# Optimization experiments

Measured on AMD Instinct MI355X. Metric: run time of the kernel, lower is better.

Reference implementation:

```python
import jax, jax.numpy as jnp
import numpy as np

KS = 3      # kernel_size
PAD = 1     # zero padding applied to x before sampling
STRIDE = 1  # stride of p_conv and final conv (as written in the repo)


def conv2d(x, w, b=None, stride=1, padding=0):
    out = jax.lax.conv_general_dilated(
        x, w, (stride, stride), [(padding, padding), (padding, padding)],
        dimension_numbers=("NCHW", "OIHW", "NCHW"))
    if b is not None:
        out = out + b[None, :, None, None]
    return out


def setup_inputs() -> dict:
    key = jax.random.key(0)
    k1, k2, k3, k4 = jax.random.split(key, 4)
    bsz, inc, outc, H, W = 4, 64, 128, 128, 128
    N = KS * KS
    x = jax.random.normal(k1, (bsz, inc, H, W), dtype=jnp.float32)
    # p_conv: Conv2d(inc, 2*ks*ks, 3, padding=1) with bias (small weights -> modest offsets)
    w_p = jax.random.normal(k2, (2 * N, inc, 3, 3), dtype=jnp.float32) * 0.02
    b_p = jax.random.normal(k3, (2 * N,), dtype=jnp.float32) * 0.1
    # final conv: Conv2d(inc, outc, ks, stride=stride, bias=None)
    w_conv = jax.random.normal(k4, (outc, inc, KS, KS), dtype=jnp.float32) * 0.05
    return {"x": x, "w_p": w_p, "b_p": b_p, "w_conv": w_conv}


def deform_conv_forward(x, w_p, b_p, w_conv):
    ks, pad, stride = KS, PAD, STRIDE
    offset = conv2d(x, w_p, b_p, stride=stride, padding=1)  # (b, 2N, oh, ow)
    N = offset.shape[1] // 2
    bsz, c, _, _ = x.shape
    oh, ow = offset.shape[2], offset.shape[3]
    xp = jnp.pad(x, ((0, 0), (0, 0), (pad, pad), (pad, pad)))
    Hp, Wp = xp.shape[2], xp.shape[3]

    # p_n: kernel-grid offsets, order matches torch.meshgrid 'ij' then flatten
    r = jnp.arange(-(ks - 1) // 2, (ks - 1) // 2 + 1, dtype=x.dtype)
    pnx, pny = jnp.meshgrid(r, r, indexing="ij")
    p_n = jnp.concatenate([pnx.ravel(), pny.ravel()])[None, :, None, None]  # (1,2N,1,1)

    # p_0: base sampling coordinates (1-indexed into padded image)
    i0 = jnp.arange(1, oh * stride + 1, stride, dtype=x.dtype)
    j0 = jnp.arange(1, ow * stride + 1, stride, dtype=x.dtype)
    p0x = jnp.broadcast_to(i0[:, None], (oh, ow))[None, None]
    p0y = jnp.broadcast_to(j0[None, :], (oh, ow))[None, None]
    p_0 = jnp.concatenate([jnp.tile(p0x, (1, N, 1, 1)), jnp.tile(p0y, (1, N, 1, 1))], axis=1)

    p = (p_0 + p_n + offset).transpose(0, 2, 3, 1)  # (b, oh, ow, 2N)

    q_lt_f = jnp.floor(p)
    q_rb_f = q_lt_f + 1.0

    def clamp_q(q):
        return jnp.concatenate(
            [jnp.clip(q[..., :N], 0, Hp - 1), jnp.clip(q[..., N:], 0, Wp - 1)],
            axis=-1).astype(jnp.int32)

    q_lt = clamp_q(q_lt_f)
    q_rb = clamp_q(q_rb_f)
    q_lb = jnp.concatenate([q_lt[..., :N], q_rb[..., N:]], axis=-1)
    q_rt = jnp.concatenate([q_rb[..., :N], q_lt[..., N:]], axis=-1)

    # clamp p itself (indices are detached in torch; gradients flow only through p here)
    p = jnp.concatenate(
        [jnp.clip(p[..., :N], 0, Hp - 1), jnp.clip(p[..., N:], 0, Wp - 1)], axis=-1)
    px, py = p[..., :N], p[..., N:]

    qf = lambda q: q.astype(x.dtype)
    g_lt = (1 + (qf(q_lt[..., :N]) - px)) * (1 + (qf(q_lt[..., N:]) - py))
    g_rb = (1 - (qf(q_rb[..., :N]) - px)) * (1 - (qf(q_rb[..., N:]) - py))
    g_lb = (1 + (qf(q_lb[..., :N]) - px)) * (1 - (qf(q_lb[..., N:]) - py))
    g_rt = (1 - (qf(q_rt[..., :N]) - px)) * (1 + (qf(q_rt[..., N:]) - py))

    x_flat = xp.reshape(bsz, c, Hp * Wp)

    def get_x_q(q):
        idx = q[..., :N] * Wp + q[..., N:]                     # (b, oh, ow, N)
        idxf = jnp.broadcast_to(idx.reshape(bsz, 1, -1), (bsz, c, oh * ow * N))
        return jnp.take_along_axis(x_flat, idxf, axis=2).reshape(bsz, c, oh, ow, N)

    x_off = (g_lt[:, None] * get_x_q(q_lt) + g_rb[:, None] * get_x_q(q_rb)
             + g_lb[:, None] * get_x_q(q_lb) + g_rt[:, None] * get_x_q(q_rt))

    # _reshape_x_offset: (b,c,oh,ow,ks*ks) -> (b,c,oh*ks,ow*ks)
    x_off = x_off.reshape(bsz, c, oh, ow, ks, ks).transpose(0, 1, 2, 4, 3, 5)
    x_off = x_off.reshape(bsz, c, oh * ks, ow * ks)

    return conv2d(x_off, w_conv, None, stride=stride, padding=0)


def reference(x, w_p, b_p, w_conv):
    return deform_conv_forward(x, w_p, b_p, w_conv)
```

## Files before the change

kernel.cpp:

```cpp
#include <hip/hip_runtime.h>
#include <hip/hip_bf16.h>

#define B_   4
#define IC   64
#define OC   128
#define HH   128
#define WW   128
#define HP   130
#define XOF  384
#define XPAD 388
#define OH2  382

typedef __attribute__((ext_vector_type(4))) float f32x4;
typedef __attribute__((ext_vector_type(8))) __bf16 bf16x8;
typedef __attribute__((ext_vector_type(8))) unsigned short us8;
typedef __attribute__((ext_vector_type(4), aligned(4))) float f32x4u;

__device__ __forceinline__ void gload16(const void* gsrc, void* ldst) {
    __builtin_amdgcn_global_load_lds(
        (const __attribute__((address_space(1))) void*)gsrc,
        (__attribute__((address_space(3))) void*)ldst, 16, 0, 0);
}

#define WAITV(N) asm volatile("s_waitcnt vmcnt(" #N ")" ::: "memory")

__device__ __forceinline__ float bf2f(unsigned short u) {
    union { unsigned int i; float f; } v; v.i = ((unsigned int)u) << 16; return v.f;
}
__device__ __forceinline__ unsigned short f2bf(float f) {
    __hip_bfloat16 h = __float2bfloat16(f);
    return reinterpret_cast<unsigned short&>(h);
}

__global__ __launch_bounds__(256) void prologue(const float* __restrict__ x,
                                                const float* __restrict__ w_p,
                                                const float* __restrict__ b_p,
                                                const float* __restrict__ wc,
                                                float* __restrict__ off,
                                                unsigned short* __restrict__ xt,
                                                unsigned short* __restrict__ Bt) {
    __shared__ __align__(16) char smem[18432];
    int bid = blockIdx.x;
    int tid = threadIdx.x;

    if (bid < 2048) {
        unsigned short (*tile)[34] = (unsigned short(*)[34])smem;
        int xt4 = bid & 3;
        int y   = (bid >> 2) & 127;
        int b   = bid >> 9;
        int x0  = xt4 * 32;

        int xl = tid & 31;
        int c8 = tid >> 5;
#pragma unroll
        for (int it = 0; it < 8; ++it) {
            int c = it * 8 + c8;
            tile[c][xl] = f2bf(x[(((size_t)b * IC + c) * HH + y) * WW + x0 + xl]);
        }
        __syncthreads();
        int c2 = (tid & 31) * 2;
#pragma unroll
        for (int it = 0; it < 4; ++it) {
            int xx = (tid >> 5) + it * 8;
            ushort2 v = { tile[c2][xx], tile[c2 + 1][xx] };
            *(ushort2*)(xt + (((size_t)b * HH + y) * WW + x0 + xx) * IC + c2) = v;
        }
    } else if (bid < 3072) {
        float (*part)[64][18] = (float(*)[64][18])smem;
        int obid = bid - 2048;
        int pxl = tid & 63;
        int icq = tid >> 6;
        int seg = obid & 1;
        int row = obid >> 1;
        int py  = row & 127;
        int b   = row >> 7;
        int px  = seg * 64 + pxl;
        int ic0 = __builtin_amdgcn_readfirstlane(icq << 4);

        float acc[18];
#pragma unroll
        for (int co = 0; co < 18; ++co) acc[co] = 0.f;

        const float* xb = x + ((size_t)b * IC + ic0) * HH * WW;

        for (int ci = 0; ci < 16; ++ci) {
            const float* xc = xb + (size_t)ci * HH * WW;
            float xv[9];
#pragma unroll
            for (int ky = 0; ky < 3; ++ky) {
                int yy = py + ky - 1;
                bool yok = (yy >= 0) && (yy < HH);
#pragma unroll
                for (int kx = 0; kx < 3; ++kx) {
                    int xx = px + kx - 1;
                    bool ok = yok && (xx >= 0) && (xx < WW);
                    xv[ky * 3 + kx] = ok ? xc[yy * WW + xx] : 0.f;
                }
            }
#pragma unroll
            for (int co = 0; co < 18; ++co) {
                const float* wrow = w_p + ((size_t)co * IC + ic0 + ci) * 9;
                f32x4u w0 = *(const f32x4u*)wrow;
                f32x4u w1 = *(const f32x4u*)(wrow + 4);
                float  w8 = wrow[8];
                acc[co] = fmaf(w0.x, xv[0], acc[co]);
                acc[co] = fmaf(w0.y, xv[1], acc[co]);
                acc[co] = fmaf(w0.z, xv[2], acc[co]);
                acc[co] = fmaf(w0.w, xv[3], acc[co]);
                acc[co] = fmaf(w1.x, xv[4], acc[co]);
                acc[co] = fmaf(w1.y, xv[5], acc[co]);
                acc[co] = fmaf(w1.z, xv[6], acc[co]);
                acc[co] = fmaf(w1.w, xv[7], acc[co]);
                acc[co] = fmaf(w8,   xv[8], acc[co]);
            }
        }

#pragma unroll
        for (int co = 0; co < 18; ++co) part[icq][pxl][co] = acc[co];
        __syncthreads();

        for (int co = icq; co < 18; co += 4) {
            float s = b_p[co] + part[0][pxl][co] + part[1][pxl][co]
                              + part[2][pxl][co] + part[3][pxl][co];
            off[((size_t)b * 18 + co) * HH * WW + (size_t)py * WW + px] = s;
        }
    } else {
        int t = (bid - 3072) * 256 + tid;
        if (t < 18 * 4 * 128 * 8) {
            int e  = t & 7;
            int oc = (t >> 3) & 127;
            int kg = (t >> 10) & 3;
            int s  = t >> 12;
            int ic = ((s & 1) << 5) + (kg << 3) + e;
            int kpos = s >> 1;
            int ky = kpos / 3, kx = kpos % 3;
            Bt[t] = f2bf(wc[(((size_t)oc * IC + ic) * 3 + ky) * 3 + kx]);
        }
    }
}

__global__ __launch_bounds__(256) void sample_nhwc(const unsigned short* __restrict__ xt,
                                                   const float* __restrict__ off,
                                                   unsigned short* __restrict__ xoff,
                                                   int b0, int nwg) {
    int orig = blockIdx.x;
    int chunk = nwg >> 3;
    int wg = (orig & 7) * chunk + (orig >> 3);

    int xtile = wg % 12;
    int tmp = wg / 12;
    int yy  = tmp % XOF;
    int bl  = tmp / XOF;
    int b   = b0 + bl;
    int xx0 = xtile * 32;

    int t  = threadIdx.x;
    int xl = t & 31;
    int cg = t >> 5;
    int xx = xx0 + xl;

    int j = xx / 3, kw = xx % 3;
    int i = yy / 3, kh = yy % 3;
    int n = kh * 3 + kw;

    const float* offb = off + (size_t)b * 18 * HH * WW + (size_t)i * WW + j;
    float offr = offb[(size_t)n * HH * WW];
    float offc = offb[(size_t)(n + 9) * HH * WW];

    float pr = (float)(i + kh) + offr;
    float pc = (float)(j + kw) + offc;

    float r0f = floorf(pr), c0f = floorf(pc);
    int r0 = min(max((int)r0f, 0), HP - 1);
    int c0 = min(max((int)c0f, 0), HP - 1);
    int r1 = min(max((int)(r0f + 1.f), 0), HP - 1);
    int c1 = min(max((int)(c0f + 1.f), 0), HP - 1);

    float prc = fminf(fmaxf(pr, 0.f), (float)(HP - 1));
    float pcc = fminf(fmaxf(pc, 0.f), (float)(HP - 1));

    float R0 = 1.f + ((float)r0 - prc);
    float R1 = 1.f - ((float)r1 - prc);
    float C0 = 1.f + ((float)c0 - pcc);
    float C1 = 1.f - ((float)c1 - pcc);

    int rr0 = r0 - 1, cc0 = c0 - 1, rr1 = r1 - 1, cc1 = c1 - 1;
    if (!(rr0 >= 0 && rr0 < HH)) R0 = 0.f;
    if (!(rr1 >= 0 && rr1 < HH)) R1 = 0.f;
    float C0m = (cc0 >= 0 && cc0 < WW) ? C0 : 0.f;
    float C1m = (cc1 >= 0 && cc1 < WW) ? C1 : 0.f;
    int ra0 = min(max(rr0, 0), HH - 1);
    int ra1 = min(max(rr1, 0), HH - 1);
    int ca0 = min(max(cc0, 0), WW - 1);
    int ca1 = min(max(cc1, 0), WW - 1);

    const unsigned short* xb = xt + (size_t)b * HH * WW * IC + cg * 8;
    us8 a  = *(const us8*)(xb + ((size_t)ra0 * WW + ca0) * IC);
    us8 bb = *(const us8*)(xb + ((size_t)ra0 * WW + ca1) * IC);
    us8 cc = *(const us8*)(xb + ((size_t)ra1 * WW + ca0) * IC);
    us8 dd = *(const us8*)(xb + ((size_t)ra1 * WW + ca1) * IC);

    us8 res;
#pragma unroll
    for (int e = 0; e < 8; ++e) {
        float v = R0 * (C0m * bf2f(a[e]) + C1m * bf2f(bb[e])) +
                  R1 * (C0m * bf2f(cc[e]) + C1m * bf2f(dd[e]));
        res[e] = f2bf(v);
    }

    size_t di = ((((size_t)bl * XOF + yy) * 8 + cg) * XPAD + xx) * 8;
    *(us8*)(xoff + di) = res;
}

__global__ __launch_bounds__(256) void conv2_mfma(const unsigned short* __restrict__ xoff,
                                                  const unsigned short* __restrict__ Bt,
                                                  float* __restrict__ out,
                                                  int b0, int nwg) {
    __shared__ __align__(16) char lds[40960];

    int orig = blockIdx.x;
    int q = nwg >> 3, r = nwg & 7;
    int xcd = orig & 7, loc = orig >> 3;
    int wgid = (xcd < r ? xcd * (q + 1) : r * (q + 1) + (xcd - r) * q) + loc;

    int xt  = wgid % 3;
    int tmp = wgid / 3;
    int oy  = tmp % OH2;
    int bl  = tmp / OH2;
    int x0  = xt << 7;

    int tid  = threadIdx.x;
    int wave = tid >> 6, lane = tid & 63;
    int wm = wave >> 1;
    int wn = wave & 1;
    int lr = lane & 15, lc = lane >> 4;

    const char* xb = (const char*)xoff + (size_t)bl * ((size_t)XOF * 8 * XPAD * 16);
    const char* bt = (const char*)Bt;

    f32x4 acc[4][4];
#pragma unroll
    for (int mf = 0; mf < 4; ++mf)
#pragma unroll
        for (int nf = 0; nf < 4; ++nf)
            acc[mf][nf] = (f32x4){0.f, 0.f, 0.f, 0.f};

    auto stageA = [&](int abuf, int s6, int third) {
        int ky  = s6 >> 1;
        int ich = s6 & 1;
        int L   = third * 4 + wave;
        int cg  = L / 3, seg = L % 3;
        const char* src = xb +
            (((size_t)(oy + ky) * 8 + ich * 4 + cg) * XPAD + x0 + seg * 64 + lane) * 16;
        char* dst = lds + abuf * 12288 + (cg * 192 + seg * 64) * 16;
        gload16(src, dst);
    };
    auto stageA_full = [&](int abuf, int s6) {
#pragma unroll
        for (int qq = 0; qq < 3; ++qq) {
            int ky  = s6 >> 1;
            int ich = s6 & 1;
            int L   = wave * 3 + qq;
            int cg  = L / 3, seg = L % 3;
            const char* src = xb +
                (((size_t)(oy + ky) * 8 + ich * 4 + cg) * XPAD + x0 + seg * 64 + lane) * 16;
            char* dst = lds + abuf * 12288 + (cg * 192 + seg * 64) * 16;
            gload16(src, dst);
        }
    };
    auto stageB = [&](int bbuf, int t) {
        int s6 = t / 3, kx = t % 3;
        int sB = ((s6 >> 1) * 3 + kx) * 2 + (s6 & 1);
        const char* bsrc = bt + (size_t)sB * 8192;
#pragma unroll
        for (int g2 = 0; g2 < 2; ++g2) {
            int g = wave * 2 + g2;
            gload16(bsrc + (size_t)g * 1024 + lane * 16,
                    lds + 24576 + bbuf * 8192 + g * 1024);
        }
    };

    auto compute = [&](int abuf, int bbuf, int kx) {
        const char* abase = lds + abuf * 12288;
        const char* bbase = lds + 24576 + bbuf * 8192;
        bf16x8 af[4], bfr[4];
#pragma unroll
        for (int mf = 0; mf < 4; ++mf)
            af[mf] = *(const bf16x8*)(abase +
                (lc * 192 + wm * 64 + mf * 16 + lr + kx) * 16);
#pragma unroll
        for (int nf = 0; nf < 4; ++nf)
            bfr[nf] = *(const bf16x8*)(bbase +
                (lc * 128 + wn * 64 + nf * 16 + lr) * 16);
        __builtin_amdgcn_s_setprio(1);
#pragma unroll
        for (int mf = 0; mf < 4; ++mf)
#pragma unroll
            for (int nf = 0; nf < 4; ++nf)
                acc[mf][nf] = __builtin_amdgcn_mfma_f32_16x16x32_bf16(
                    af[mf], bfr[nf], acc[mf][nf], 0, 0, 0);
        __builtin_amdgcn_s_setprio(0);
    };

    stageA_full(0, 0);
    stageB(0, 0);

    int abuf = 0, bbuf = 0;
#pragma unroll
    for (int s6 = 0; s6 < 6; ++s6) {
#pragma unroll
        for (int kx = 0; kx < 3; ++kx) {
            const int t = s6 * 3 + kx;
            if (t + 1 < 18) stageB(bbuf ^ 1, t + 1);
            if (s6 + 1 < 6) stageA(abuf ^ 1, s6 + 1, kx);
            if (s6 < 5)          { WAITV(3); }
            else if (kx < 2)     { WAITV(2); }
            else                 { WAITV(0); }
            __builtin_amdgcn_s_barrier();
            __builtin_amdgcn_sched_barrier(0);
            compute(abuf, bbuf, kx);
            __builtin_amdgcn_sched_barrier(0);
            __builtin_amdgcn_s_barrier();
            bbuf ^= 1;
        }
        abuf ^= 1;
    }

    int b = b0 + bl;
#pragma unroll
    for (int mf = 0; mf < 4; ++mf) {
        int ox0 = x0 + wm * 64 + mf * 16 + (lc << 2);
#pragma unroll
        for (int nf = 0; nf < 4; ++nf) {
            int oc = wn * 64 + nf * 16 + lr;
            float* po = out + (((size_t)b * OC + oc) * OH2 + oy) * OH2 + ox0;
            if (ox0 + 3 < OH2) {
                *(f32x4u*)po = acc[mf][nf];
            } else {
#pragma unroll
                for (int rr = 0; rr < 4; ++rr)
                    if (ox0 + rr < OH2) po[rr] = acc[mf][nf][rr];
            }
        }
    }
}

extern "C" void kernel_launch(void* const* d_in, const int* in_sizes, int n_in,
                              void* d_out, int out_size, void* d_ws, size_t ws_size,
                              hipStream_t stream) {
    const float* x      = (const float*)d_in[0];
    const float* w_p    = (const float*)d_in[1];
    const float* b_p    = (const float*)d_in[2];
    const float* w_conv = (const float*)d_in[3];
    float* out = (float*)d_out;

    const size_t offElems = (size_t)B_ * 18 * HH * WW;
    const size_t xtElems  = (size_t)B_ * HH * WW * IC;
    const size_t btElems  = (size_t)18 * 4 * 128 * 8;
    const size_t xofElems = (size_t)XOF * 8 * XPAD * 8;
    const size_t slack    = 16384;

    float* off = (float*)d_ws;
    unsigned short* xtb  = (unsigned short*)(off + offElems);
    unsigned short* Bt   = xtb + xtElems;
    unsigned short* xoff = Bt + btElems;

    const size_t headBytes = offElems * 4 + (xtElems + btElems) * 2;
    const bool allBatch = ws_size >= headBytes + 4 * xofElems * 2 + slack;

    prologue<<<3360, 256, 0, stream>>>(x, w_p, b_p, w_conv, off, xtb, Bt);

    if (allBatch) {
        int snwg = 12 * XOF * B_;
        sample_nhwc<<<snwg, 256, 0, stream>>>(xtb, off, xoff, 0, snwg);
        int cnwg = 3 * OH2 * B_;
        conv2_mfma<<<cnwg, 256, 0, stream>>>(xoff, Bt, out, 0, cnwg);
    } else {
        for (int b = 0; b < B_; ++b) {
            int snwg = 12 * XOF;
            sample_nhwc<<<snwg, 256, 0, stream>>>(xtb, off, xoff, b, snwg);
            int cnwg = 3 * OH2;
            conv2_mfma<<<cnwg, 256, 0, stream>>>(xoff, Bt, out, b, cnwg);
        }
    }
}
```

Baseline: 228.5 us.

## Load MFMA operands directly from global memory into registers, dropping LDS staging

Removes the LDS double-buffered staging (global_load_lds plus barriers) in the main implicit-GEMM conv kernel. Each wave now loads its A and B fragments straight from global memory into registers, ping-ponging two register sets so the next loads are issued while the current MFMAs run. This removes barriers and LDS traffic, but each wave re-fetches data that was previously shared across waves. It also relies on the caches to absorb the overlapping kx-shifted A reads, and uses more vector registers.

```diff
diff --git a/kernel.cpp b/kernel.cpp
--- a/kernel.cpp
+++ b/kernel.cpp
@@ -15,14 +15,6 @@
 typedef __attribute__((ext_vector_type(8))) __bf16 bf16x8;
 typedef __attribute__((ext_vector_type(8))) unsigned short us8;
 typedef __attribute__((ext_vector_type(4), aligned(4))) float f32x4u;
-
-__device__ __forceinline__ void gload16(const void* gsrc, void* ldst) {
-    __builtin_amdgcn_global_load_lds(
-        (const __attribute__((address_space(1))) void*)gsrc,
-        (__attribute__((address_space(3))) void*)ldst, 16, 0, 0);
-}
-
-#define WAITV(N) asm volatile("s_waitcnt vmcnt(" #N ")" ::: "memory")
 
 __device__ __forceinline__ float bf2f(unsigned short u) {
     union { unsigned int i; float f; } v; v.i = ((unsigned int)u) << 16; return v.f;
@@ -216,8 +208,6 @@
                                                   const unsigned short* __restrict__ Bt,
                                                   float* __restrict__ out,
                                                   int b0, int nwg) {
-    __shared__ __align__(16) char lds[40960];
-
     int orig = blockIdx.x;
     int q = nwg >> 3, r = nwg & 7;
     int xcd = orig & 7, loc = orig >> 3;
@@ -236,7 +226,11 @@
     int lr = lane & 15, lc = lane >> 4;
 
     const char* xb = (const char*)xoff + (size_t)bl * ((size_t)XOF * 8 * XPAD * 16);
+    const char* baseA = xb + ((size_t)oy * 8 * XPAD + x0) * 16;
     const char* bt = (const char*)Bt;
+
+    const int voffA = (lc * XPAD + wm * 64 + lr) * 16;
+    const int voffB = (lc * 128 + wn * 64 + lr) * 16;
 
     f32x4 acc[4][4];
 #pragma unroll
@@ -245,85 +239,42 @@
         for (int nf = 0; nf < 4; ++nf)
             acc[mf][nf] = (f32x4){0.f, 0.f, 0.f, 0.f};
 
-    auto stageA = [&](int abuf, int s6, int third) {
-        int ky  = s6 >> 1;
-        int ich = s6 & 1;
-        int L   = third * 4 + wave;
-        int cg  = L / 3, seg = L % 3;
-        const char* src = xb +
-            (((size_t)(oy + ky) * 8 + ich * 4 + cg) * XPAD + x0 + seg * 64 + lane) * 16;
-        char* dst = lds + abuf * 12288 + (cg * 192 + seg * 64) * 16;
-        gload16(src, dst);
+    auto loadA = [&](bf16x8* af, int t) {
+        const int ky = t / 6, ich = (t / 3) & 1, kx = t % 3;
+        const char* p = baseA + ((size_t)(ky * 8 + ich * 4) * XPAD + kx) * 16 + voffA;
+#pragma unroll
+        for (int mf = 0; mf < 4; ++mf)
+            af[mf] = *(const bf16x8*)(p + mf * 256);
     };
-    auto stageA_full = [&](int abuf, int s6) {
-#pragma unroll
-        for (int qq = 0; qq < 3; ++qq) {
-            int ky  = s6 >> 1;
-            int ich = s6 & 1;
-            int L   = wave * 3 + qq;
-            int cg  = L / 3, seg = L % 3;
-            const char* src = xb +
-                (((size_t)(oy + ky) * 8 + ich * 4 + cg) * XPAD + x0 + seg * 64 + lane) * 16;
-            char* dst = lds + abuf * 12288 + (cg * 192 + seg * 64) * 16;
-            gload16(src, dst);
-        }
+    auto loadB = [&](bf16x8* bf, int t) {
+        const int s6 = t / 3, kx = t % 3;
+        const int sB = ((s6 >> 1) * 3 + kx) * 2 + (s6 & 1);
+        const char* p = bt + (size_t)sB * 8192 + voffB;
+#pragma unroll
+        for (int nf = 0; nf < 4; ++nf)
+            bf[nf] = *(const bf16x8*)(p + nf * 256);
     };
-    auto stageB = [&](int bbuf, int t) {
-        int s6 = t / 3, kx = t % 3;
-        int sB = ((s6 >> 1) * 3 + kx) * 2 + (s6 & 1);
-        const char* bsrc = bt + (size_t)sB * 8192;
-#pragma unroll
-        for (int g2 = 0; g2 < 2; ++g2) {
-            int g = wave * 2 + g2;
-            gload16(bsrc + (size_t)g * 1024 + lane * 16,
-                    lds + 24576 + bbuf * 8192 + g * 1024);
-        }
-    };
-
-    auto compute = [&](int abuf, int bbuf, int kx) {
-        const char* abase = lds + abuf * 12288;
-        const char* bbase = lds + 24576 + bbuf * 8192;
-        bf16x8 af[4], bfr[4];
-#pragma unroll
-        for (int mf = 0; mf < 4; ++mf)
-            af[mf] = *(const bf16x8*)(abase +
-                (lc * 192 + wm * 64 + mf * 16 + lr + kx) * 16);
-#pragma unroll
-        for (int nf = 0; nf < 4; ++nf)
-            bfr[nf] = *(const bf16x8*)(bbase +
-                (lc * 128 + wn * 64 + nf * 16 + lr) * 16);
+    auto domfma = [&](const bf16x8* af, const bf16x8* bf) {
         __builtin_amdgcn_s_setprio(1);
 #pragma unroll
         for (int mf = 0; mf < 4; ++mf)
 #pragma unroll
             for (int nf = 0; nf < 4; ++nf)
                 acc[mf][nf] = __builtin_amdgcn_mfma_f32_16x16x32_bf16(
-                    af[mf], bfr[nf], acc[mf][nf], 0, 0, 0);
+                    af[mf], bf[nf], acc[mf][nf], 0, 0, 0);
         __builtin_amdgcn_s_setprio(0);
     };
 
-    stageA_full(0, 0);
-    stageB(0, 0);
-
-    int abuf = 0, bbuf = 0;
-#pragma unroll
-    for (int s6 = 0; s6 < 6; ++s6) {
-#pragma unroll
-        for (int kx = 0; kx < 3; ++kx) {
-            const int t = s6 * 3 + kx;
-            if (t + 1 < 18) stageB(bbuf ^ 1, t + 1);
-            if (s6 + 1 < 6) stageA(abuf ^ 1, s6 + 1, kx);
-            if (s6 < 5)          { WAITV(3); }
-            else if (kx < 2)     { WAITV(2); }
-            else                 { WAITV(0); }
-            __builtin_amdgcn_s_barrier();
-            __builtin_amdgcn_sched_barrier(0);
-            compute(abuf, bbuf, kx);
-            __builtin_amdgcn_sched_barrier(0);
-            __builtin_amdgcn_s_barrier();
-            bbuf ^= 1;
-        }
-        abuf ^= 1;
+    bf16x8 aA[4], bA[4], aB[4], bB[4];
+    loadA(aA, 0); loadB(bA, 0);
+
+#pragma unroll
+    for (int tt = 0; tt < 9; ++tt) {
+        const int t0 = 2 * tt;
+        loadA(aB, t0 + 1); loadB(bB, t0 + 1);
+        domfma(aA, bA);
+        if (t0 + 2 < 18) { loadA(aA, t0 + 2); loadB(bA, t0 + 2); }
+        domfma(aB, bB);
     }
 
     int b = b0 + bl;
```

After: 234.9 us. +2.8%, slower.

## Triple-buffer B tiles and issue loads after barrier, one barrier per step

Applied to the files above, without the earlier changes.

Changes the conv2 MFMA main loop from double-buffered B with two barriers per step to a triple-buffered B ring, prefetching two steps ahead. Each step now has a single barrier, and the A tile for the next ky/channel slice is loaded in one burst at kx==0 instead of spread across three steps. The goal is to cut barrier stalls and hide global-to-LDS latency better. In exchange LDS use grows from 40 KB to 48 KB, which may lower occupancy, and the vmcnt accounting is more fragile.

```diff
diff --git a/kernel.cpp b/kernel.cpp
--- a/kernel.cpp
+++ b/kernel.cpp
@@ -216,7 +216,7 @@
                                                   const unsigned short* __restrict__ Bt,
                                                   float* __restrict__ out,
                                                   int b0, int nwg) {
-    __shared__ __align__(16) char lds[40960];
+    __shared__ __align__(16) char lds[49152];
 
     int orig = blockIdx.x;
     int q = nwg >> 3, r = nwg & 7;
@@ -245,16 +245,6 @@
         for (int nf = 0; nf < 4; ++nf)
             acc[mf][nf] = (f32x4){0.f, 0.f, 0.f, 0.f};
 
-    auto stageA = [&](int abuf, int s6, int third) {
-        int ky  = s6 >> 1;
-        int ich = s6 & 1;
-        int L   = third * 4 + wave;
-        int cg  = L / 3, seg = L % 3;
-        const char* src = xb +
-            (((size_t)(oy + ky) * 8 + ich * 4 + cg) * XPAD + x0 + seg * 64 + lane) * 16;
-        char* dst = lds + abuf * 12288 + (cg * 192 + seg * 64) * 16;
-        gload16(src, dst);
-    };
     auto stageA_full = [&](int abuf, int s6) {
 #pragma unroll
         for (int qq = 0; qq < 3; ++qq) {
@@ -268,21 +258,22 @@
             gload16(src, dst);
         }
     };
-    auto stageB = [&](int bbuf, int t) {
+    auto stageB = [&](int t) {
         int s6 = t / 3, kx = t % 3;
         int sB = ((s6 >> 1) * 3 + kx) * 2 + (s6 & 1);
+        int buf = t % 3;
         const char* bsrc = bt + (size_t)sB * 8192;
 #pragma unroll
         for (int g2 = 0; g2 < 2; ++g2) {
             int g = wave * 2 + g2;
             gload16(bsrc + (size_t)g * 1024 + lane * 16,
-                    lds + 24576 + bbuf * 8192 + g * 1024);
+                    lds + 24576 + buf * 8192 + g * 1024);
         }
     };
 
-    auto compute = [&](int abuf, int bbuf, int kx) {
+    auto compute = [&](int abuf, int t, int kx) {
         const char* abase = lds + abuf * 12288;
-        const char* bbase = lds + 24576 + bbuf * 8192;
+        const char* bbase = lds + 24576 + (t % 3) * 8192;
         bf16x8 af[4], bfr[4];
 #pragma unroll
         for (int mf = 0; mf < 4; ++mf)
@@ -303,27 +294,22 @@
     };
 
     stageA_full(0, 0);
-    stageB(0, 0);
-
-    int abuf = 0, bbuf = 0;
-#pragma unroll
-    for (int s6 = 0; s6 < 6; ++s6) {
-#pragma unroll
-        for (int kx = 0; kx < 3; ++kx) {
-            const int t = s6 * 3 + kx;
-            if (t + 1 < 18) stageB(bbuf ^ 1, t + 1);
-            if (s6 + 1 < 6) stageA(abuf ^ 1, s6 + 1, kx);
-            if (s6 < 5)          { WAITV(3); }
-            else if (kx < 2)     { WAITV(2); }
-            else                 { WAITV(0); }
-            __builtin_amdgcn_s_barrier();
-            __builtin_amdgcn_sched_barrier(0);
-            compute(abuf, bbuf, kx);
-            __builtin_amdgcn_sched_barrier(0);
-            __builtin_amdgcn_s_barrier();
-            bbuf ^= 1;
-        }
-        abuf ^= 1;
+    stageB(0);
+    stageB(1);
+
+#pragma unroll
+    for (int t = 0; t < 18; ++t) {
+        const int kx = t % 3, s6 = t / 3;
+        const int n = (t == 17) ? 0 : ((t % 3 == 1 && t < 15) ? 5 : 2);
+        if (n == 0)      { WAITV(0); }
+        else if (n == 2) { WAITV(2); }
+        else             { WAITV(5); }
+        __builtin_amdgcn_s_barrier();
+        __builtin_amdgcn_sched_barrier(0);
+        if (t + 2 < 18) stageB(t + 2);
+        if (kx == 0 && s6 + 1 < 6) stageA_full((s6 & 1) ^ 1, s6 + 1);
+        compute(s6 & 1, t, kx);
+        __builtin_amdgcn_sched_barrier(0);
     }
 
     int b = b0 + bl;
```

After: 217.7 us. 1.05x faster.
